# Kernel optimization log

Measured on AMD Instinct MI355X. Metric: run time of the kernel, lower is better.

The kernel has to match this reference:

```python
import jax, jax.numpy as jnp
import numpy as np

B, S, D, H, L, V, FFM = 4, 2048, 512, 8, 6, 8000, 4
HD = D // H
FF = FFM * D


def setup_inputs() -> dict:
    key = jax.random.key(0)
    ks = jax.random.split(key, 12)
    sc = 0.02
    return {
        "tokens": jax.random.randint(ks[0], (B, S), 0, V),
        "embed": jax.random.normal(ks[1], (V, D), jnp.float32) * sc,
        "wq": jax.random.normal(ks[2], (L, D, D), jnp.float32) * sc,
        "wk": jax.random.normal(ks[3], (L, D, D), jnp.float32) * sc,
        "wv": jax.random.normal(ks[4], (L, D, D), jnp.float32) * sc,
        "wo": jax.random.normal(ks[5], (L, D, D), jnp.float32) * sc,
        "bo": jnp.zeros((L, D), jnp.float32),
        "w1": jax.random.normal(ks[6], (L, D, FF), jnp.float32) * sc,
        "b1": jnp.zeros((L, FF), jnp.float32),
        "w2": jax.random.normal(ks[7], (L, FF, D), jnp.float32) * sc,
        "b2": jnp.zeros((L, D), jnp.float32),
        "ln_g": jnp.ones((L, D), jnp.float32),
        "ln_b": jnp.zeros((L, D), jnp.float32),
        "lnf_g": jnp.ones((D,), jnp.float32),
        "lnf_b": jnp.zeros((D,), jnp.float32),
        "w_out": jax.random.normal(ks[8], (D, V), jnp.float32) * sc,
        "b_out": jnp.zeros((V,), jnp.float32),
    }


def _layernorm(x, g, b, eps=1e-5):
    m = jnp.mean(x, -1, keepdims=True)
    v = jnp.var(x, -1, keepdims=True)
    return (x - m) * jax.lax.rsqrt(v + eps) * g + b


def _pos_encoding():
    pos = jnp.arange(S, dtype=jnp.float32)[:, None]
    div = jnp.exp(jnp.arange(0, D, 2, dtype=jnp.float32) * (-np.log(10000.0) / D))
    pe = jnp.zeros((S, D), jnp.float32)
    pe = pe.at[:, 0::2].set(jnp.sin(pos * div))
    pe = pe.at[:, 1::2].set(jnp.cos(pos * div))
    return pe


def _forward(tokens, embed, wq, wk, wv, wo, bo, w1, b1, w2, b2, ln_g, ln_b,
             lnf_g, lnf_b, w_out, b_out):
    x = embed[tokens] + _pos_encoding()[None]  # [B,S,D]
    causal = jnp.tril(jnp.ones((S, S), bool))
    neg_inf = jnp.float32(-jnp.inf)
    # NOTE: original scales scores by 1/sqrt(n_embd) (key.weight.size(-1) == D)
    inv_scale = 1.0 / jnp.sqrt(jnp.float32(D))

    def block(x, p):
        pwq, pwk, pwv, pwo, pbo, pw1, pb1, pw2, pb2, g, b = p
        # attention sublayer (same LayerNorm params used for both sublayers,
        # matching the repo's reuse of add_and_norm_1)
        h = _layernorm(x, g, b)
        q = (h @ pwq).reshape(B, S, H, HD)
        k = (h @ pwk).reshape(B, S, H, HD)
        v = (h @ pwv).reshape(B, S, H, HD)
        scores = jnp.einsum('bqhd,bkhd->bhqk', q, k) * inv_scale
        scores = jnp.where(causal, scores, neg_inf)
        att = jax.nn.softmax(scores, axis=-1)
        o = jnp.einsum('bhqk,bkhd->bqhd', att, v).reshape(B, S, D)
        x = x + o @ pwo + pbo
        # FFN sublayer
        h2 = _layernorm(x, g, b)
        x = x + jax.nn.relu(h2 @ pw1 + pb1) @ pw2 + pb2
        return x, None

    params = (wq, wk, wv, wo, bo, w1, b1, w2, b2, ln_g, ln_b)
    x, _ = jax.lax.scan(block, x, params)
    x = _layernorm(x, lnf_g, lnf_b)
    logits = x @ w_out + b_out  # [B,S,V]
    return logits


def reference(tokens, embed, wq, wk, wv, wo, bo, w1, b1, w2, b2, ln_g, ln_b,
              lnf_g, lnf_b, w_out, b_out):
    return _forward(tokens, embed, wq, wk, wv, wo, bo, w1, b1, w2, b2,
                    ln_g, ln_b, lnf_g, lnf_b, w_out, b_out)
```

## Files before the change

kernel.cpp:

```cpp
#include <hip/hip_runtime.h>

#define Bsz 4
#define Ssz 2048
#define Dsz 512
#define Hsz 8
#define Lsz 6
#define Vsz 8000
#define FFsz 2048
#define Msz (Bsz*Ssz)
#define VszPad 8192

typedef unsigned short u16;
typedef unsigned int u32;
typedef __attribute__((ext_vector_type(8))) short bf16x8;
typedef __attribute__((ext_vector_type(4))) float f32x4;
typedef __attribute__((ext_vector_type(16))) float f32x16;
typedef __attribute__((ext_vector_type(4))) u32 u32x4;
typedef __attribute__((ext_vector_type(4))) u16 u16x4;

__device__ __forceinline__ u16 f2b(float f) {
    union { float f; unsigned u; } x; x.f = f;
    return (u16)((x.u + 0x7fffu + ((x.u >> 16) & 1u)) >> 16);
}
__device__ __forceinline__ float b2f(u16 v) {
    union { u32 u; float f; } x; x.u = ((u32)v) << 16; return x.f;
}

#define GLOAD_LDS16(g, l) __builtin_amdgcn_global_load_lds( \
    (const __attribute__((address_space(1))) u32*)(g), \
    (__attribute__((address_space(3))) u32*)(l), 16, 0, 0)

__global__ __launch_bounds__(256) void embed_kernel(const int* __restrict__ tokens,
                                                    const float* __restrict__ embed,
                                                    u16* __restrict__ x) {
    int idx = blockIdx.x * 256 + threadIdx.x;
    int row = idx >> 8, p = idx & 255;
    int tok = tokens[row];
    int s = row & (Ssz - 1);
    float div = __expf((float)p * (-9.210340371976184f / 256.f));
    float ang = (float)s * div;
    float2 e = ((const float2*)(embed + (size_t)tok * Dsz))[p];
    u32 o = (u32)f2b(e.x + sinf(ang)) | ((u32)f2b(e.y + cosf(ang)) << 16);
    ((u32*)(x + (size_t)row * Dsz))[p] = o;
}

__global__ __launch_bounds__(256) void ln_kernel(const u16* __restrict__ x,
                                                 const float* __restrict__ g,
                                                 const float* __restrict__ bta,
                                                 u16* __restrict__ out) {
    int wave = threadIdx.x >> 6, lane = threadIdx.x & 63;
    int row = blockIdx.x * 4 + wave;
    bf16x8 a = ((const bf16x8*)(x + (size_t)row * Dsz))[lane];
    float vals[8];
    #pragma unroll
    for (int i = 0; i < 8; ++i) vals[i] = b2f((u16)a[i]);
    float s = 0.f;
    #pragma unroll
    for (int i = 0; i < 8; ++i) s += vals[i];
    #pragma unroll
    for (int o = 32; o; o >>= 1) s += __shfl_xor(s, o);
    float mean = s * (1.f / 512.f);
    float sq = 0.f;
    #pragma unroll
    for (int i = 0; i < 8; ++i) { float d = vals[i] - mean; sq += d * d; }
    #pragma unroll
    for (int o = 32; o; o >>= 1) sq += __shfl_xor(sq, o);
    float rstd = rsqrtf(sq * (1.f / 512.f) + 1e-5f);
    int base = lane * 8;
    bf16x8 rv;
    #pragma unroll
    for (int i = 0; i < 8; ++i)
        rv[i] = (short)f2b((vals[i] - mean) * rstd * g[base + i] + bta[base + i]);
    *(bf16x8*)(out + (size_t)row * Dsz + base) = rv;
}

__global__ __launch_bounds__(256) void tconv_kernel(const float* __restrict__ src,
                                                    u16* __restrict__ dst,
                                                    int R, int C,
                                                    size_t sstride, size_t dstride) {
    __shared__ float tile[32][33];
    const float* s = src + blockIdx.z * sstride;
    u16* d = dst + blockIdx.z * dstride;
    int c0 = blockIdx.x * 32, r0 = blockIdx.y * 32;
    int tx = threadIdx.x & 31, ty = threadIdx.x >> 5;
    #pragma unroll
    for (int i = 0; i < 32; i += 8)
        tile[ty + i][tx] = s[(size_t)(r0 + ty + i) * C + c0 + tx];
    __syncthreads();
    #pragma unroll
    for (int i = 0; i < 32; i += 8)
        d[(size_t)(c0 + ty + i) * R + r0 + tx] = f2b(tile[tx][ty + i]);
}

template<bool BIAS, bool RES, bool RELU, bool OF32, bool OBF16, bool XN, int BMF>
__global__ __launch_bounds__(256, 4) void gemm_kernel(const u16* __restrict__ A,
                                                   const u16* __restrict__ BT,
                                                   const float* __restrict__ bias,
                                                   const u16* __restrict__ res,
                                                   float* __restrict__ outf,
                                                   u16* __restrict__ outb,
                                                   int M, int N, int K) {
    __shared__ u16 As[BMF * 32 * 64];
    __shared__ u16 Bs[128 * 64];
    int tid = threadIdx.x;
    int wave = tid >> 6, lane = tid & 63;
    int wm = wave >> 1, wn = wave & 1;
    int gx = gridDim.x;
    int bid = blockIdx.y * gx + blockIdx.x;
    int xcd = bid & 7, j = bid >> 3;
    int mblk, nblk;
    if (XN) { mblk = j >> 3; nblk = xcd * 8 + (j & 7); }
    else    { int sm = gridDim.y >> 3; mblk = xcd * sm + j / gx; nblk = j % gx; }
    int m0 = mblk * (BMF * 32), n0 = nblk * 128;
    int lr = lane & 15, lg = lane >> 4;
    int srow = lane >> 3;
    int scol = (lane & 7) * 8;
    f32x4 acc[BMF][4] = {};
    for (int k0 = 0; k0 < K; k0 += 64) {
        #pragma unroll
        for (int i = 0; i < BMF; ++i) {
            int chunk = wave * BMF + i;
            int r = chunk * 8 + srow;
            GLOAD_LDS16(A + (size_t)(m0 + r) * K + k0 + scol, &As[chunk * 512]);
        }
        #pragma unroll
        for (int i = 0; i < 4; ++i) {
            int chunk = wave * 4 + i;
            int r = chunk * 8 + srow;
            GLOAD_LDS16(BT + (size_t)(n0 + r) * K + k0 + scol, &Bs[chunk * 512]);
        }
        __syncthreads();
        #pragma unroll
        for (int kk = 0; kk < 2; ++kk) {
            bf16x8 af[BMF], bfr[4];
            #pragma unroll
            for (int m = 0; m < BMF; ++m)
                af[m] = *(const bf16x8*)(As + (wm * (BMF * 16) + m * 16 + lr) * 64 + kk * 32 + lg * 8);
            #pragma unroll
            for (int n = 0; n < 4; ++n)
                bfr[n] = *(const bf16x8*)(Bs + (wn * 64 + n * 16 + lr) * 64 + kk * 32 + lg * 8);
            #pragma unroll
            for (int m = 0; m < BMF; ++m)
                #pragma unroll
                for (int n = 0; n < 4; ++n)
                    acc[m][n] = __builtin_amdgcn_mfma_f32_16x16x32_bf16(af[m], bfr[n], acc[m][n], 0, 0, 0);
        }
        __syncthreads();
    }
    #pragma unroll
    for (int m = 0; m < BMF; ++m) {
        int row = m0 + wm * (BMF * 16) + m * 16 + lg * 4;
        #pragma unroll
        for (int n = 0; n < 4; ++n) {
            int col = n0 + wn * 64 + n * 16 + lr;
            if (col < N) {
                float bv = BIAS ? bias[col] : 0.f;
                #pragma unroll
                for (int j2 = 0; j2 < 4; ++j2) {
                    float v = acc[m][n][j2] + bv;
                    if (RES) v += b2f(res[(size_t)(row + j2) * N + col]);
                    if (RELU) v = fmaxf(v, 0.f);
                    if (OF32) outf[(size_t)(row + j2) * N + col] = v;
                    if (OBF16) outb[(size_t)(row + j2) * N + col] = f2b(v);
                }
            }
        }
    }
}

template<bool BIAS, bool RELU, bool OF32, bool OBF16, int MAP, bool QKV>
__global__ __launch_bounds__(512, 2) void gemm256_kernel(const u16* __restrict__ A,
                                                         const u16* __restrict__ BT,
                                                         const float* __restrict__ bias,
                                                         float* __restrict__ outf,
                                                         u16* __restrict__ outb,
                                                         u16* __restrict__ vT,
                                                         int M, int N, int K) {
    __shared__ u16 As[256 * 64];
    __shared__ u16 Bs[256 * 64];
    int tid = threadIdx.x;
    int wid = tid >> 6, lane = tid & 63;
    int wr = wid >> 2, wc = wid & 3;
    int lr = lane & 15, lg = lane >> 4;
    int bid = blockIdx.y * gridDim.x + blockIdx.x;
    int xcd = bid & 7, j = bid >> 3;
    int mblk, nblk;
    if (MAP == 0) { int npx = gridDim.x >> 3; if (npx < 1) npx = 1;
                    nblk = xcd * npx + j % npx; mblk = j / npx; }
    else          { int mpx = gridDim.y >> 3;
                    mblk = xcd * mpx + j / gridDim.x; nblk = j % gridDim.x; }
    int m0 = mblk * 256, n0 = nblk * 256;
    int grow = tid >> 3;
    int gcol = (tid & 7) * 8;
    f32x4 acc[8][4] = {};
    for (int k0 = 0; k0 < K; k0 += 64) {
        #pragma unroll
        for (int i = 0; i < 4; ++i) {
            int r = i * 64 + grow;
            GLOAD_LDS16(A + (size_t)(m0 + r) * K + k0 + gcol, &As[(i * 64 + wid * 8) * 64]);
            GLOAD_LDS16(BT + (size_t)(n0 + r) * K + k0 + gcol, &Bs[(i * 64 + wid * 8) * 64]);
        }
        __syncthreads();
        #pragma unroll
        for (int kk = 0; kk < 2; ++kk) {
            bf16x8 af[8], bfr[4];
            #pragma unroll
            for (int m = 0; m < 8; ++m)
                af[m] = *(const bf16x8*)(As + (wr * 128 + m * 16 + lr) * 64 + kk * 32 + lg * 8);
            #pragma unroll
            for (int n = 0; n < 4; ++n)
                bfr[n] = *(const bf16x8*)(Bs + (wc * 64 + n * 16 + lr) * 64 + kk * 32 + lg * 8);
            #pragma unroll
            for (int m = 0; m < 8; ++m)
                #pragma unroll
                for (int n = 0; n < 4; ++n)
                    acc[m][n] = __builtin_amdgcn_mfma_f32_16x16x32_bf16(af[m], bfr[n], acc[m][n], 0, 0, 0);
        }
        __syncthreads();
    }
    #pragma unroll
    for (int m = 0; m < 8; ++m) {
        int row = m0 + wr * 128 + m * 16 + lg * 4;
        #pragma unroll
        for (int n = 0; n < 4; ++n) {
            int col = n0 + wc * 64 + n * 16 + lr;
            if (QKV && col >= 1024) {
                int hd = col - 1024;
                int hh = hd >> 6; hd &= 63;
                int b = row >> 11, s = row & 2047;
                u16x4 v4;
                #pragma unroll
                for (int j2 = 0; j2 < 4; ++j2) v4[j2] = f2b(acc[m][n][j2]);
                *(u16x4*)(vT + ((size_t)(b * 8 + hh) * 64 + hd) * Ssz + s) = v4;
            } else if (col < N) {
                float bv = BIAS ? bias[col] : 0.f;
                #pragma unroll
                for (int j2 = 0; j2 < 4; ++j2) {
                    float v = acc[m][n][j2] + bv;
                    if (RELU) v = fmaxf(v, 0.f);
                    if (OF32) outf[(size_t)(row + j2) * N + col] = v;
                    if (OBF16) outb[(size_t)(row + j2) * N + col] = f2b(v);
                }
            }
        }
    }
}

__global__ __launch_bounds__(256, 2) void flash5_kernel(const u16* __restrict__ qkv,
                                                        const u16* __restrict__ vT,
                                                        u16* __restrict__ o) {
    __shared__ u16 Ks[2][64 * 64];
    __shared__ u16 Vs[2][64 * 64];
    int blk = blockIdx.x;
    int bh = blk & 31;
    int c = 15 - (blk >> 5);
    int b = bh >> 3, hh = bh & 7;
    int tid = threadIdx.x, wave = tid >> 6, lane = tid & 63;
    int l31 = lane & 31, h5 = lane >> 5;
    int g = c * 4 + wave;
    int qg = g * 32 + l31;
    int ext = (g >> 1) + 1;
    int nt = 2 * c + 2;
    const float cs = 0.044194173824159216f;

    bf16x8 qf[4];
    {
        const u16* qrow = qkv + (size_t)(b * Ssz + qg) * 1536 + hh * 64;
        #pragma unroll
        for (int cb = 0; cb < 4; ++cb)
            qf[cb] = *(const bf16x8*)(qrow + cb * 16 + h5 * 8);
    }
    f32x16 Oa0 = {}, Oa1 = {};
    float m_run = -1e30f, l_run = 0.f;
    int sr = tid >> 3;
    int sc2 = (tid & 7) * 8;
    const u16* kbase = qkv + (size_t)(b * Ssz) * 1536 + 512 + hh * 64;
    const u16* vbase = vT + (size_t)bh * 64 * Ssz;
    int byteA = (sr * 128 + sc2 * 2) ^ ((sr & 7) << 4);
    int byteB = ((sr + 32) * 128 + sc2 * 2) ^ ((sr & 7) << 4);

    {
        bf16x8 kA = *(const bf16x8*)(kbase + (size_t)sr * 1536 + sc2);
        bf16x8 kB = *(const bf16x8*)(kbase + (size_t)(32 + sr) * 1536 + sc2);
        bf16x8 vA = *(const bf16x8*)(vbase + (size_t)sr * Ssz + sc2);
        bf16x8 vB = *(const bf16x8*)(vbase + (size_t)(32 + sr) * Ssz + sc2);
        *(bf16x8*)((char*)Ks[0] + byteA) = kA;
        *(bf16x8*)((char*)Ks[0] + byteB) = kB;
        *(bf16x8*)((char*)Vs[0] + byteA) = vA;
        *(bf16x8*)((char*)Vs[0] + byteB) = vB;
    }
    __syncthreads();

    for (int kt = 0; kt < nt; ++kt) {
        int cur = kt & 1;
        bool pf = (kt + 1 < nt);
        bf16x8 kA, kB, vA, vB;
        if (pf) {
            kA = *(const bf16x8*)(kbase + (size_t)((kt + 1) * 64 + sr) * 1536 + sc2);
            kB = *(const bf16x8*)(kbase + (size_t)((kt + 1) * 64 + 32 + sr) * 1536 + sc2);
            vA = *(const bf16x8*)(vbase + (size_t)sr * Ssz + (kt + 1) * 64 + sc2);
            vB = *(const bf16x8*)(vbase + (size_t)(32 + sr) * Ssz + (kt + 1) * 64 + sc2);
        }
        const u16* Kc = Ks[cur];
        const u16* Vc = Vs[cur];
        if (kt < ext) {
            bool dtile = (kt == ext - 1);
            int mts = (dtile && !(g & 1)) ? 1 : 2;
            f32x16 st[2] = {};
            __builtin_amdgcn_s_setprio(1);
            #pragma unroll
            for (int mt = 0; mt < 2; ++mt)
                if (mt < mts) {
                    int r = mt * 32 + l31;
                    #pragma unroll
                    for (int cb = 0; cb < 4; ++cb) {
                        int byte = (r * 128 + (cb * 16 + h5 * 8) * 2) ^ ((r & 7) << 4);
                        bf16x8 kf = *(const bf16x8*)((char*)Kc + byte);
                        st[mt] = __builtin_amdgcn_mfma_f32_32x32x16_bf16(kf, qf[cb], st[mt], 0, 0, 0);
                    }
                }
            __builtin_amdgcn_s_setprio(0);
            float pmax = -1e30f;
            #pragma unroll
            for (int mt = 0; mt < 2; ++mt)
                if (mt < mts)
                    #pragma unroll
                    for (int r = 0; r < 16; ++r) {
                        float v = st[mt][r];
                        if (dtile) {
                            int kglob = kt * 64 + mt * 32 + (r & 3) + 8 * (r >> 2) + 4 * h5;
                            if (kglob > qg) v = -1e30f;
                        }
                        st[mt][r] = v;
                        pmax = fmaxf(pmax, v);
                    }
            pmax = fmaxf(pmax, __shfl_xor(pmax, 32));
            if (!__all(pmax - m_run <= 181.019336f)) {
                float mn = fmaxf(m_run, pmax);
                float al = __expf((m_run - mn) * cs);
                l_run *= al;
                #pragma unroll
                for (int r = 0; r < 16; ++r) {
                    int qloc = (r & 3) + 8 * (r >> 2) + 4 * h5;
                    float alr = __shfl(al, qloc);
                    Oa0[r] *= alr; Oa1[r] *= alr;
                }
                m_run = mn;
            }
            float ls = 0.f;
            u32 pk[2][8];
            #pragma unroll
            for (int mt = 0; mt < 2; ++mt)
                if (mt < mts)
                    #pragma unroll
                    for (int w = 0; w < 8; ++w) {
                        float p0 = __expf((st[mt][2 * w]     - m_run) * cs);
                        float p1 = __expf((st[mt][2 * w + 1] - m_run) * cs);
                        ls += p0 + p1;
                        pk[mt][w] = (u32)f2b(p0) | ((u32)f2b(p1) << 16);
                    }
            l_run += ls + __shfl_xor(ls, 32);
            __builtin_amdgcn_s_setprio(1);
            #pragma unroll
            for (int mt = 0; mt < 2; ++mt)
                if (mt < mts) {
                    u32 pko[8];
                    #pragma unroll
                    for (int w = 0; w < 8; ++w)
                        pko[w] = __shfl_xor(pk[mt][w], 32);
                    #pragma unroll
                    for (int kbl = 0; kbl < 2; ++kbl) {
                        int kb = mt * 2 + kbl;
                        u32x4 aw;
                        #pragma unroll
                        for (int w = 0; w < 4; ++w) {
                            int widx = 4 * kbl + 2 * h5 + (w & 1);
                            bool own = (w < 2) != (h5 == 1);
                            aw[w] = own ? pk[mt][widx] : pko[widx];
                        }
                        bf16x8 af = __builtin_bit_cast(bf16x8, aw);
                        #pragma unroll
                        for (int dt = 0; dt < 2; ++dt) {
                            int r = dt * 32 + l31;
                            int byte = (r * 128 + (kb * 16 + h5 * 8) * 2) ^ ((r & 7) << 4);
                            bf16x8 vf = *(const bf16x8*)((char*)Vc + byte);
                            if (dt == 0) Oa0 = __builtin_amdgcn_mfma_f32_32x32x16_bf16(af, vf, Oa0, 0, 0, 0);
                            else         Oa1 = __builtin_amdgcn_mfma_f32_32x32x16_bf16(af, vf, Oa1, 0, 0, 0);
                        }
                    }
                }
            __builtin_amdgcn_s_setprio(0);
        }
        if (pf) {
            u16* Kn = Ks[cur ^ 1];
            u16* Vn = Vs[cur ^ 1];
            *(bf16x8*)((char*)Kn + byteA) = kA;
            *(bf16x8*)((char*)Kn + byteB) = kB;
            *(bf16x8*)((char*)Vn + byteA) = vA;
            *(bf16x8*)((char*)Vn + byteB) = vB;
        }
        __syncthreads();
    }
    float rln = 1.f / l_run;
    u16* obase = o + (size_t)(b * Ssz) * Dsz + hh * 64;
    #pragma unroll
    for (int r = 0; r < 16; ++r) {
        int qloc = (r & 3) + 8 * (r >> 2) + 4 * h5;
        float s = __shfl(rln, qloc);
        u16* orow = obase + (size_t)(g * 32 + qloc) * Dsz + l31;
        orow[0]  = f2b(Oa0[r] * s);
        orow[32] = f2b(Oa1[r] * s);
    }
}

extern "C" void kernel_launch(void* const* d_in, const int* in_sizes, int n_in,
                              void* d_out, int out_size, void* d_ws, size_t ws_size,
                              hipStream_t stream) {
    (void)in_sizes; (void)n_in; (void)out_size; (void)ws_size;
    const int*   tokens = (const int*)d_in[0];
    const float* embed  = (const float*)d_in[1];
    const float* wq     = (const float*)d_in[2];
    const float* wk     = (const float*)d_in[3];
    const float* wv     = (const float*)d_in[4];
    const float* wo     = (const float*)d_in[5];
    const float* bo     = (const float*)d_in[6];
    const float* w1     = (const float*)d_in[7];
    const float* b1     = (const float*)d_in[8];
    const float* w2     = (const float*)d_in[9];
    const float* b2     = (const float*)d_in[10];
    const float* ln_g   = (const float*)d_in[11];
    const float* ln_b   = (const float*)d_in[12];
    const float* lnf_g  = (const float*)d_in[13];
    const float* lnf_b  = (const float*)d_in[14];
    const float* w_out  = (const float*)d_in[15];
    const float* b_out  = (const float*)d_in[16];
    float* out = (float*)d_out;

    char* ws = (char*)d_ws;
    size_t off = 0;
    auto alloc = [&](size_t bytes) {
        void* p = ws + off;
        off += (bytes + 255) & ~(size_t)255;
        return p;
    };
    u16*   x     = (u16*)alloc((size_t)Msz * Dsz * 2);
    u16*   h     = (u16*)alloc((size_t)Msz * Dsz * 2);
    u16*   qkv   = (u16*)alloc((size_t)Msz * 1536 * 2);
    u16*   vT    = (u16*)alloc((size_t)Bsz * Hsz * 64 * Ssz * 2);
    u16*   ob    = (u16*)alloc((size_t)Msz * Dsz * 2);
    u16*   ffh   = (u16*)alloc((size_t)Msz * FFsz * 2);
    u16*   wqkvT = (u16*)alloc((size_t)Lsz * 3 * Dsz * Dsz * 2);
    u16*   woT   = (u16*)alloc((size_t)Lsz * Dsz * Dsz * 2);
    u16*   w1T   = (u16*)alloc((size_t)Lsz * FFsz * Dsz * 2);
    u16*   w2T   = (u16*)alloc((size_t)Lsz * Dsz * FFsz * 2);
    u16*   w_outT= (u16*)alloc((size_t)VszPad * Dsz * 2);

    dim3 tb(256);
    size_t dd = (size_t)Dsz * Dsz;
    hipMemsetAsync(w_outT + (size_t)Vsz * Dsz, 0, (size_t)(VszPad - Vsz) * Dsz * 2, stream);
    tconv_kernel<<<dim3(16, 16, Lsz), tb, 0, stream>>>(wq, wqkvT + 0 * dd, Dsz, Dsz, dd, 3 * dd);
    tconv_kernel<<<dim3(16, 16, Lsz), tb, 0, stream>>>(wk, wqkvT + 1 * dd, Dsz, Dsz, dd, 3 * dd);
    tconv_kernel<<<dim3(16, 16, Lsz), tb, 0, stream>>>(wv, wqkvT + 2 * dd, Dsz, Dsz, dd, 3 * dd);
    tconv_kernel<<<dim3(16, 16, Lsz), tb, 0, stream>>>(wo, woT, Dsz, Dsz, dd, dd);
    tconv_kernel<<<dim3(64, 16, Lsz), tb, 0, stream>>>(w1, w1T, Dsz, FFsz, (size_t)Dsz * FFsz, (size_t)FFsz * Dsz);
    tconv_kernel<<<dim3(16, 64, Lsz), tb, 0, stream>>>(w2, w2T, FFsz, Dsz, (size_t)FFsz * Dsz, (size_t)Dsz * FFsz);
    tconv_kernel<<<dim3(250, 16, 1), tb, 0, stream>>>(w_out, w_outT, Dsz, Vsz, 0, 0);

    embed_kernel<<<Msz * 256 / 256, tb, 0, stream>>>(tokens, embed, x);

    for (int l = 0; l < Lsz; ++l) {
        ln_kernel<<<Msz / 4, tb, 0, stream>>>(x, ln_g + l * Dsz, ln_b + l * Dsz, h);
        gemm256_kernel<false, false, false, true, 1, true><<<dim3(6, Msz / 256), dim3(512), 0, stream>>>(
            h, wqkvT + (size_t)l * 3 * dd, nullptr, nullptr, qkv, vT, Msz, 1536, Dsz);
        flash5_kernel<<<dim3(512), tb, 0, stream>>>(qkv, vT, ob);
        gemm_kernel<true, true, false, false, true, false, 2><<<dim3(4, Msz / 64), tb, 0, stream>>>(
            ob, woT + (size_t)l * dd, bo + l * Dsz, x, nullptr, x, Msz, Dsz, Dsz);
        ln_kernel<<<Msz / 4, tb, 0, stream>>>(x, ln_g + l * Dsz, ln_b + l * Dsz, h);
        gemm256_kernel<true, true, false, true, 0, false><<<dim3(FFsz / 256, Msz / 256), dim3(512), 0, stream>>>(
            h, w1T + (size_t)l * FFsz * Dsz, b1 + l * FFsz, nullptr, ffh, nullptr, Msz, FFsz, Dsz);
        gemm_kernel<true, true, false, false, true, false, 2><<<dim3(4, Msz / 64), tb, 0, stream>>>(
            ffh, w2T + (size_t)l * Dsz * FFsz, b2 + l * Dsz, x, nullptr, x, Msz, Dsz, FFsz);
    }
    ln_kernel<<<Msz / 4, tb, 0, stream>>>(x, lnf_g, lnf_b, h);
    gemm256_kernel<true, false, true, false, 0, false><<<dim3(VszPad / 256, Msz / 256), dim3(512), 0, stream>>>(
        h, w_outT, b_out, out, nullptr, nullptr, Msz, Vsz, Dsz);
}
```

Baseline: 1.690 ms.

## Replace 256x256 GEMM with smaller-tile kernels and fuse QKV weight conversion

Removes the 256x256-tile GEMM and routes the QKV projection through the 256-thread gemm_kernel (BMF=4, with the V-transpose epilogue moved in). The FFN-up and output-projection GEMMs now use a new 256x128-tile, 512-thread kernel. It also merges the three Q/K/V weight-transpose launches into one, raises flash-attention occupancy to 3 blocks per SM, and switches some bf16 conversions to the library intrinsic. Smaller tiles give more blocks and better load balance, at the cost of less data reuse per block and more register pressure in the attention kernel.

```diff
diff --git a/kernel.cpp b/kernel.cpp
--- a/kernel.cpp
+++ b/kernel.cpp
@@ -1,4 +1,5 @@
 #include <hip/hip_runtime.h>
+#include <hip/hip_bf16.h>
 
 #define Bsz 4
 #define Ssz 2048
@@ -21,6 +22,10 @@
 __device__ __forceinline__ u16 f2b(float f) {
     union { float f; unsigned u; } x; x.f = f;
     return (u16)((x.u + 0x7fffu + ((x.u >> 16) & 1u)) >> 16);
+}
+__device__ __forceinline__ u16 f2bn(float f) {
+    __hip_bfloat16 h = __float2bfloat16(f);
+    return __builtin_bit_cast(u16, h);
 }
 __device__ __forceinline__ float b2f(u16 v) {
     union { u32 u; float f; } x; x.u = ((u32)v) << 16; return x.f;
@@ -92,13 +97,33 @@
         d[(size_t)(c0 + ty + i) * R + r0 + tx] = f2b(tile[tx][ty + i]);
 }
 
-template<bool BIAS, bool RES, bool RELU, bool OF32, bool OBF16, bool XN, int BMF>
+__global__ __launch_bounds__(256) void tconvqkv_kernel(const float* __restrict__ wq,
+                                                       const float* __restrict__ wk,
+                                                       const float* __restrict__ wv,
+                                                       u16* __restrict__ dst) {
+    __shared__ float tile[32][33];
+    int z = blockIdx.z, which = z / Lsz, l = z % Lsz;
+    const float* s = (which == 0 ? wq : which == 1 ? wk : wv) + (size_t)l * Dsz * Dsz;
+    u16* d = dst + ((size_t)l * 3 + which) * Dsz * Dsz;
+    int c0 = blockIdx.x * 32, r0 = blockIdx.y * 32;
+    int tx = threadIdx.x & 31, ty = threadIdx.x >> 5;
+    #pragma unroll
+    for (int i = 0; i < 32; i += 8)
+        tile[ty + i][tx] = s[(size_t)(r0 + ty + i) * Dsz + c0 + tx];
+    __syncthreads();
+    #pragma unroll
+    for (int i = 0; i < 32; i += 8)
+        d[(size_t)(c0 + ty + i) * Dsz + r0 + tx] = f2b(tile[tx][ty + i]);
+}
+
+template<bool BIAS, bool RES, bool RELU, bool OF32, bool OBF16, bool XN, int BMF, bool QKV>
 __global__ __launch_bounds__(256, 4) void gemm_kernel(const u16* __restrict__ A,
                                                    const u16* __restrict__ BT,
                                                    const float* __restrict__ bias,
                                                    const u16* __restrict__ res,
                                                    float* __restrict__ outf,
                                                    u16* __restrict__ outb,
+                                                   u16* __restrict__ vT,
                                                    int M, int N, int K) {
     __shared__ u16 As[BMF * 32 * 64];
     __shared__ u16 Bs[128 * 64];
@@ -153,77 +178,6 @@
         #pragma unroll
         for (int n = 0; n < 4; ++n) {
             int col = n0 + wn * 64 + n * 16 + lr;
-            if (col < N) {
-                float bv = BIAS ? bias[col] : 0.f;
-                #pragma unroll
-                for (int j2 = 0; j2 < 4; ++j2) {
-                    float v = acc[m][n][j2] + bv;
-                    if (RES) v += b2f(res[(size_t)(row + j2) * N + col]);
-                    if (RELU) v = fmaxf(v, 0.f);
-                    if (OF32) outf[(size_t)(row + j2) * N + col] = v;
-                    if (OBF16) outb[(size_t)(row + j2) * N + col] = f2b(v);
-                }
-            }
-        }
-    }
-}
-
-template<bool BIAS, bool RELU, bool OF32, bool OBF16, int MAP, bool QKV>
-__global__ __launch_bounds__(512, 2) void gemm256_kernel(const u16* __restrict__ A,
-                                                         const u16* __restrict__ BT,
-                                                         const float* __restrict__ bias,
-                                                         float* __restrict__ outf,
-                                                         u16* __restrict__ outb,
-                                                         u16* __restrict__ vT,
-                                                         int M, int N, int K) {
-    __shared__ u16 As[256 * 64];
-    __shared__ u16 Bs[256 * 64];
-    int tid = threadIdx.x;
-    int wid = tid >> 6, lane = tid & 63;
-    int wr = wid >> 2, wc = wid & 3;
-    int lr = lane & 15, lg = lane >> 4;
-    int bid = blockIdx.y * gridDim.x + blockIdx.x;
-    int xcd = bid & 7, j = bid >> 3;
-    int mblk, nblk;
-    if (MAP == 0) { int npx = gridDim.x >> 3; if (npx < 1) npx = 1;
-                    nblk = xcd * npx + j % npx; mblk = j / npx; }
-    else          { int mpx = gridDim.y >> 3;
-                    mblk = xcd * mpx + j / gridDim.x; nblk = j % gridDim.x; }
-    int m0 = mblk * 256, n0 = nblk * 256;
-    int grow = tid >> 3;
-    int gcol = (tid & 7) * 8;
-    f32x4 acc[8][4] = {};
-    for (int k0 = 0; k0 < K; k0 += 64) {
-        #pragma unroll
-        for (int i = 0; i < 4; ++i) {
-            int r = i * 64 + grow;
-            GLOAD_LDS16(A + (size_t)(m0 + r) * K + k0 + gcol, &As[(i * 64 + wid * 8) * 64]);
-            GLOAD_LDS16(BT + (size_t)(n0 + r) * K + k0 + gcol, &Bs[(i * 64 + wid * 8) * 64]);
-        }
-        __syncthreads();
-        #pragma unroll
-        for (int kk = 0; kk < 2; ++kk) {
-            bf16x8 af[8], bfr[4];
-            #pragma unroll
-            for (int m = 0; m < 8; ++m)
-                af[m] = *(const bf16x8*)(As + (wr * 128 + m * 16 + lr) * 64 + kk * 32 + lg * 8);
-            #pragma unroll
-            for (int n = 0; n < 4; ++n)
-                bfr[n] = *(const bf16x8*)(Bs + (wc * 64 + n * 16 + lr) * 64 + kk * 32 + lg * 8);
-            #pragma unroll
-            for (int m = 0; m < 8; ++m)
-                #pragma unroll
-                for (int n = 0; n < 4; ++n)
-                    acc[m][n] = __builtin_amdgcn_mfma_f32_16x16x32_bf16(af[m], bfr[n], acc[m][n], 0, 0, 0);
-        }
-        __syncthreads();
-    }
-    #pragma unroll
-    for (int m = 0; m < 8; ++m) {
-        int row = m0 + wr * 128 + m * 16 + lg * 4;
-        #pragma unroll
-        for (int n = 0; n < 4; ++n) {
-            int col = n0 + wc * 64 + n * 16 + lr;
             if (QKV && col >= 1024) {
                 int hd = col - 1024;
                 int hh = hd >> 6; hd &= 63;
@@ -237,6 +191,7 @@
                 #pragma unroll
                 for (int j2 = 0; j2 < 4; ++j2) {
                     float v = acc[m][n][j2] + bv;
+                    if (RES) v += b2f(res[(size_t)(row + j2) * N + col]);
                     if (RELU) v = fmaxf(v, 0.f);
                     if (OF32) outf[(size_t)(row + j2) * N + col] = v;
                     if (OBF16) outb[(size_t)(row + j2) * N + col] = f2b(v);
@@ -246,7 +201,79 @@
     }
 }
 
-__global__ __launch_bounds__(256, 2) void flash5_kernel(const u16* __restrict__ qkv,
+template<bool BIAS, bool RELU, bool OF32, bool XN>
+__global__ __launch_bounds__(512, 2) void gemmBig_kernel(const u16* __restrict__ A,
+                                                         const u16* __restrict__ BT,
+                                                         const float* __restrict__ bias,
+                                                         float* __restrict__ outf,
+                                                         u16* __restrict__ outb,
+                                                         int M, int N, int K) {
+    __shared__ u16 As[256 * 64];
+    __shared__ u16 Bs[128 * 64];
+    int tid = threadIdx.x;
+    int wave = tid >> 6, lane = tid & 63;
+    int wm = wave >> 1, wn = wave & 1;
+    int gx = gridDim.x;
+    int bid = blockIdx.y * gx + blockIdx.x;
+    int xcd = bid & 7, j = bid >> 3;
+    int mblk, nblk;
+    if (XN) { mblk = j >> 3; nblk = xcd * 8 + (j & 7); }
+    else    { int sm = gridDim.y >> 3; mblk = xcd * sm + j / gx; nblk = j % gx; }
+    int m0 = mblk * 256, n0 = nblk * 128;
+    int lr = lane & 15, lg = lane >> 4;
+    int srow = lane >> 3;
+    int scol = (lane & 7) * 8;
+    f32x4 acc[4][4] = {};
+    for (int k0 = 0; k0 < K; k0 += 64) {
+        #pragma unroll
+        for (int i = 0; i < 4; ++i) {
+            int chunk = wave * 4 + i;
+            GLOAD_LDS16(A + (size_t)(m0 + chunk * 8 + srow) * K + k0 + scol, &As[chunk * 512]);
+        }
+        #pragma unroll
+        for (int i = 0; i < 2; ++i) {
+            int chunk = wave * 2 + i;
+            GLOAD_LDS16(BT + (size_t)(n0 + chunk * 8 + srow) * K + k0 + scol, &Bs[chunk * 512]);
+        }
+        __syncthreads();
+        #pragma unroll
+        for (int kk = 0; kk < 2; ++kk) {
+            bf16x8 af[4], bfr[4];
+            #pragma unroll
+            for (int m = 0; m < 4; ++m)
+                af[m] = *(const bf16x8*)(As + (wm * 64 + m * 16 + lr) * 64 + kk * 32 + lg * 8);
+            #pragma unroll
+            for (int n = 0; n < 4; ++n)
+                bfr[n] = *(const bf16x8*)(Bs + (wn * 64 + n * 16 + lr) * 64 + kk * 32 + lg * 8);
+            #pragma unroll
+            for (int m = 0; m < 4; ++m)
+                #pragma unroll
+                for (int n = 0; n < 4; ++n)
+                    acc[m][n] = __builtin_amdgcn_mfma_f32_16x16x32_bf16(af[m], bfr[n], acc[m][n], 0, 0, 0);
+        }
+        __syncthreads();
+    }
+    #pragma unroll
+    for (int m = 0; m < 4; ++m) {
+        int row = m0 + wm * 64 + m * 16 + lg * 4;
+        #pragma unroll
+        for (int n = 0; n < 4; ++n) {
+            int col = n0 + wn * 64 + n * 16 + lr;
+            if (col < N) {
+                float bv = BIAS ? bias[col] : 0.f;
+                #pragma unroll
+                for (int j2 = 0; j2 < 4; ++j2) {
+                    float v = acc[m][n][j2] + bv;
+                    if (RELU) v = fmaxf(v, 0.f);
+                    if (OF32) outf[(size_t)(row + j2) * N + col] = v;
+                    else      outb[(size_t)(row + j2) * N + col] = f2b(v);
+                }
+            }
+        }
+    }
+}
+
+__global__ __launch_bounds__(256, 3) void flash5_kernel(const u16* __restrict__ qkv,
                                                         const u16* __restrict__ vT,
                                                         u16* __restrict__ o) {
     __shared__ u16 Ks[2][64 * 64];
@@ -357,7 +384,7 @@
                         float p0 = __expf((st[mt][2 * w]     - m_run) * cs);
                         float p1 = __expf((st[mt][2 * w + 1] - m_run) * cs);
                         ls += p0 + p1;
-                        pk[mt][w] = (u32)f2b(p0) | ((u32)f2b(p1) << 16);
+                        pk[mt][w] = (u32)f2bn(p0) | ((u32)f2bn(p1) << 16);
                     }
             l_run += ls + __shfl_xor(ls, 32);
             __builtin_amdgcn_s_setprio(1);
@@ -408,8 +435,8 @@
         int qloc = (r & 3) + 8 * (r >> 2) + 4 * h5;
         float s = __shfl(rln, qloc);
         u16* orow = obase + (size_t)(g * 32 + qloc) * Dsz + l31;
-        orow[0]  = f2b(Oa0[r] * s);
-        orow[32] = f2b(Oa1[r] * s);
+        orow[0]  = f2bn(Oa0[r] * s);
+        orow[32] = f2bn(Oa1[r] * s);
     }
 }
 
@@ -458,9 +485,7 @@
     dim3 tb(256);
     size_t dd = (size_t)Dsz * Dsz;
     hipMemsetAsync(w_outT + (size_t)Vsz * Dsz, 0, (size_t)(VszPad - Vsz) * Dsz * 2, stream);
-    tconv_kernel<<<dim3(16, 16, Lsz), tb, 0, stream>>>(wq, wqkvT + 0 * dd, Dsz, Dsz, dd, 3 * dd);
-    tconv_kernel<<<dim3(16, 16, Lsz), tb, 0, stream>>>(wk, wqkvT + 1 * dd, Dsz, Dsz, dd, 3 * dd);
-    tconv_kernel<<<dim3(16, 16, Lsz), tb, 0, stream>>>(wv, wqkvT + 2 * dd, Dsz, Dsz, dd, 3 * dd);
+    tconvqkv_kernel<<<dim3(16, 16, Lsz * 3), tb, 0, stream>>>(wq, wk, wv, wqkvT);
     tconv_kernel<<<dim3(16, 16, Lsz), tb, 0, stream>>>(wo, woT, Dsz, Dsz, dd, dd);
     tconv_kernel<<<dim3(64, 16, Lsz), tb, 0, stream>>>(w1, w1T, Dsz, FFsz, (size_t)Dsz * FFsz, (size_t)FFsz * Dsz);
     tconv_kernel<<<dim3(16, 64, Lsz), tb, 0, stream>>>(w2, w2T, FFsz, Dsz, (size_t)FFsz * Dsz, (size_t)Dsz * FFsz);
@@ -470,18 +495,18 @@
 
     for (int l = 0; l < Lsz; ++l) {
         ln_kernel<<<Msz / 4, tb, 0, stream>>>(x, ln_g + l * Dsz, ln_b + l * Dsz, h);
-        gemm256_kernel<false, false, false, true, 1, true><<<dim3(6, Msz / 256), dim3(512), 0, stream>>>(
-            h, wqkvT + (size_t)l * 3 * dd, nullptr, nullptr, qkv, vT, Msz, 1536, Dsz);
+        gemm_kernel<false, false, false, false, true, false, 4, true><<<dim3(12, Msz / 128), tb, 0, stream>>>(
+            h, wqkvT + (size_t)l * 3 * dd, nullptr, nullptr, nullptr, qkv, vT, Msz, 1536, Dsz);
         flash5_kernel<<<dim3(512), tb, 0, stream>>>(qkv, vT, ob);
-        gemm_kernel<true, true, false, false, true, false, 2><<<dim3(4, Msz / 64), tb, 0, stream>>>(
-            ob, woT + (size_t)l * dd, bo + l * Dsz, x, nullptr, x, Msz, Dsz, Dsz);
+        gemm_kernel<true, true, false, false, true, false, 2, false><<<dim3(4, Msz / 64), tb, 0, stream>>>(
+            ob, woT + (size_t)l * dd, bo + l * Dsz, x, nullptr, x, nullptr, Msz, Dsz, Dsz);
         ln_kernel<<<Msz / 4, tb, 0, stream>>>(x, ln_g + l * Dsz, ln_b + l * Dsz, h);
-        gemm256_kernel<true, true, false, true, 0, false><<<dim3(FFsz / 256, Msz / 256), dim3(512), 0, stream>>>(
-            h, w1T + (size_t)l * FFsz * Dsz, b1 + l * FFsz, nullptr, ffh, nullptr, Msz, FFsz, Dsz);
-        gemm_kernel<true, true, false, false, true, false, 2><<<dim3(4, Msz / 64), tb, 0, stream>>>(
-            ffh, w2T + (size_t)l * Dsz * FFsz, b2 + l * Dsz, x, nullptr, x, Msz, Dsz, FFsz);
+        gemmBig_kernel<true, true, false, false><<<dim3(16, Msz / 256), dim3(512), 0, stream>>>(
+            h, w1T + (size_t)l * FFsz * Dsz, b1 + l * FFsz, nullptr, ffh, Msz, FFsz, Dsz);
+        gemm_kernel<true, true, false, false, true, false, 2, false><<<dim3(4, Msz / 64), tb, 0, stream>>>(
+            ffh, w2T + (size_t)l * Dsz * FFsz, b2 + l * Dsz, x, nullptr, x, nullptr, Msz, Dsz, FFsz);
     }
     ln_kernel<<<Msz / 4, tb, 0, stream>>>(x, lnf_g, lnf_b, h);
-    gemm256_kernel<true, false, true, false, 0, false><<<dim3(VszPad / 256, Msz / 256), dim3(512), 0, stream>>>(
-        h, w_outT, b_out, out, nullptr, nullptr, Msz, Vsz, Dsz);
-}
+    gemmBig_kernel<true, false, true, true><<<dim3(64, Msz / 256), dim3(512), 0, stream>>>(
+        h, w_outT, b_out, out, nullptr, Msz, Vsz, Dsz);
+}
```

Result: faster. 1.548 ms (-8.4%).
